# Kernel tuning notes

Measured on AMD Instinct MI355X. Metric: run time of the kernel, lower is better.

The kernel has to match this reference:

```python
import jax, jax.numpy as jnp
import numpy as np

B = 16384       # batch of peptide samples
M = 15          # max_peptide_size
R = 64          # aa_rep_size
P = 34          # number of pocket positions
F = 9           # filter_size
A = 20          # alphabet size


def setup_inputs() -> dict:
    key = jax.random.key(0)
    k1, k2, k3, k4 = jax.random.split(key, 4)
    peptide_encoding = jax.random.normal(k1, (B, M, R), dtype=jnp.float32)
    pocket_aa_idx = jax.random.randint(k2, (B, P), 0, A, dtype=jnp.int32)
    adj_mask = jax.random.randint(k3, (B, P, M), 0, 2, dtype=jnp.int32)
    # one trainable 1-D filter of length F per alphabet letter ('uniform' init)
    kernels = jax.random.uniform(k4, (A, F), dtype=jnp.float32, minval=-0.05, maxval=0.05)
    return {"peptide_encoding": peptide_encoding, "pocket_aa_idx": pocket_aa_idx,
            "adj_mask": adj_mask, "kernels": kernels}


def reference(peptide_encoding, pocket_aa_idx, adj_mask, kernels):
    # Per pocket position p of sample b: filter = kernels[pocket_aa_idx[b,p]]  [B,P,F]
    filt = kernels[pocket_aa_idx]
    # Convolution is linear, so sum the adjacent peptide-position encodings first:
    # s[b,p,r] = sum_m adj_mask[b,p,m] * peptide_encoding[b,m,r]   -> [B,P,R]
    s = jnp.einsum('bpm,bmr->bpr', adj_mask.astype(peptide_encoding.dtype), peptide_encoding)
    # Full convolution along the representation axis: output length R + F - 1
    conv1 = jax.vmap(jax.vmap(lambda a, b: jnp.convolve(a, b, mode='full')))
    out = conv1(s, filt)  # [B, P, R+F-1]
    return out
```

## Files before the change

kernel.cpp:

```cpp
#include <hip/hip_runtime.h>

#define MM 15
#define RR 64
#define PP 34
#define FF 9
#define AA 20
#define OW 72
#define SP 84
#define KS 12
#define AJ 20
#define AJROWS 48

__global__ __launch_bounds__(256)
void ppc_kernel(const float* __restrict__ pe,
                const int*   __restrict__ idx,
                const int*   __restrict__ adj,
                const float* __restrict__ kernels,
                float*       __restrict__ out)
{
    const int b = blockIdx.x;
    const int t = threadIdx.x;

    __shared__ float s_pe[MM * RR];
    __shared__ float s_kern[AA * KS];
    __shared__ float s_adjf[AJROWS * AJ];
    __shared__ int   s_idx[PP];
    __shared__ float s_s[PP * SP];

    const float* peb  = pe  + (size_t)b * (MM * RR);
    const int*   adjb = adj + (size_t)b * (PP * MM);

    if (t < (MM * RR) / 4)
        *(float4*)&s_pe[t * 4] = *(const float4*)&peb[t * 4];
    if (t < AA * FF) {
        int a = (unsigned)t / FF, j = t - a * FF;
        s_kern[a * KS + j] = kernels[t];
    }
    for (int i = t; i < PP * MM; i += 256) {
        int p = (unsigned)i / MM, m = i - p * MM;
        s_adjf[p * AJ + m] = (float)adjb[i];
    }
    for (int i = t; i < PP * 5; i += 256) {
        int p = (unsigned)i / 5, k = i - p * 5;
        s_adjf[p * AJ + MM + k] = 0.0f;
    }
    for (int i = t; i < (AJROWS - PP) * AJ; i += 256)
        s_adjf[PP * AJ + i] = 0.0f;
    if (t < PP) s_idx[t] = idx[(size_t)b * PP + t];
    for (int i = t; i < PP * 20; i += 256) {
        int p = (unsigned)i / 20, c2 = i - p * 20;
        s_s[p * SP + (c2 < 8 ? c2 : 64 + c2)] = 0.0f;
    }
    __syncthreads();

    const int c  = t & 15;
    const int q  = t >> 4;
    const int r0 = c << 2;

    {
        const float* g0 = &s_adjf[(q)      * AJ];
        const float* g1 = &s_adjf[(q + 16) * AJ];
        const float* g2 = &s_adjf[(q + 32) * AJ];
        float x0=0,y0=0,z0=0,w0=0, x1=0,y1=0,z1=0,w1=0, x2=0,y2=0,z2=0,w2=0;
        #pragma unroll
        for (int mc = 0; mc < 4; ++mc) {
            const float4 a0 = *(const float4*)&g0[mc * 4];
            const float4 a1 = *(const float4*)&g1[mc * 4];
            const float4 a2 = *(const float4*)&g2[mc * 4];
            #pragma unroll
            for (int mm = 0; mm < 4; ++mm) {
                const int m = mc * 4 + mm;
                if (m < MM) {
                    const float4 v = *(const float4*)&s_pe[m * RR + r0];
                    const float ga = (&a0.x)[mm], gb = (&a1.x)[mm], gc = (&a2.x)[mm];
                    x0 += ga*v.x; y0 += ga*v.y; z0 += ga*v.z; w0 += ga*v.w;
                    x1 += gb*v.x; y1 += gb*v.y; z1 += gb*v.z; w1 += gb*v.w;
                    x2 += gc*v.x; y2 += gc*v.y; z2 += gc*v.z; w2 += gc*v.w;
                }
            }
        }
        *(float4*)&s_s[(q)      * SP + 8 + r0] = make_float4(x0,y0,z0,w0);
        *(float4*)&s_s[(q + 16) * SP + 8 + r0] = make_float4(x1,y1,z1,w1);
        if (q + 32 < PP)
            *(float4*)&s_s[(q + 32) * SP + 8 + r0] = make_float4(x2,y2,z2,w2);
    }
    __syncthreads();

    float* outb = out + (size_t)b * (PP * OW);

    auto do_p = [&](const int p) {
        float kf[FF];
        {
            const float* kb = &s_kern[s_idx[p] * KS];
            const float4 k0 = *(const float4*)&kb[0];
            const float4 k1 = *(const float4*)&kb[4];
            kf[0]=k0.x; kf[1]=k0.y; kf[2]=k0.z; kf[3]=k0.w;
            kf[4]=k1.x; kf[5]=k1.y; kf[6]=k1.z; kf[7]=k1.w;
            kf[8]=kb[8];
        }
        const float* row = &s_s[p * SP];
        {
            float w[12];
            *(float4*)&w[0] = *(const float4*)&row[r0];
            *(float4*)&w[4] = *(const float4*)&row[r0 + 4];
            *(float4*)&w[8] = *(const float4*)&row[r0 + 8];
            float ax=0, ay=0, az=0, aw=0;
            #pragma unroll
            for (int j = 0; j < FF; ++j) {
                const float k = kf[j];
                ax += k * w[8  - j];
                ay += k * w[9  - j];
                az += k * w[10 - j];
                aw += k * w[11 - j];
            }
            *(float4*)&outb[p * OW + r0] = make_float4(ax, ay, az, aw);
        }
        if (c < 2) {
            const int o0 = 64 + r0;
            float w[12];
            *(float4*)&w[0] = *(const float4*)&row[o0];
            *(float4*)&w[4] = *(const float4*)&row[o0 + 4];
            *(float4*)&w[8] = *(const float4*)&row[o0 + 8];
            float ax=0, ay=0, az=0, aw=0;
            #pragma unroll
            for (int j = 0; j < FF; ++j) {
                const float k = kf[j];
                ax += k * w[8  - j];
                ay += k * w[9  - j];
                az += k * w[10 - j];
                aw += k * w[11 - j];
            }
            *(float4*)&outb[p * OW + o0] = make_float4(ax, ay, az, aw);
        }
    };

    do_p(q);
    do_p(q + 16);
    if (q + 32 < PP) do_p(q + 32);
}

extern "C" void kernel_launch(void* const* d_in, const int* in_sizes, int n_in,
                              void* d_out, int out_size, void* d_ws, size_t ws_size,
                              hipStream_t stream) {
    const float* pe      = (const float*)d_in[0];
    const int*   idx     = (const int*)  d_in[1];
    const int*   adj     = (const int*)  d_in[2];
    const float* kernels = (const float*)d_in[3];
    float*       out     = (float*)d_out;

    const int B = in_sizes[0] / (MM * RR);
    ppc_kernel<<<B, 256, 0, stream>>>(pe, idx, adj, kernels, out);
}
```

Before: 72.01 us.

## Remap einsum stage to one column per thread with register-cached peptide values

The adjacency-weighted sum stage is remapped. Each thread now owns one representation column r, keeps all 15 peptide values for that column in registers, and loops over the pocket rows with wavefront-uniform (broadcast) float4 reads of the adjacency row. The adjacency padding rows and padding zeroing are removed by shrinking the row stride to 16, and the halo zeroing of s_s now uses float4 stores. The aim is fewer shared-memory loads and less setup work. The trade-off is scalar rather than vectorized s_s stores in that stage, and reduced ILP per thread.

After: 76.74 us. +6.6%, slower.

```diff
diff --git a/kernel.cpp b/kernel.cpp
--- a/kernel.cpp
+++ b/kernel.cpp
@@ -8,8 +8,7 @@
 #define OW 72
 #define SP 84
 #define KS 12
-#define AJ 20
-#define AJROWS 48
+#define AJ 16
 
 __global__ __launch_bounds__(256)
 void ppc_kernel(const float* __restrict__ pe,
@@ -23,7 +22,7 @@
 
     __shared__ float s_pe[MM * RR];
     __shared__ float s_kern[AA * KS];
-    __shared__ float s_adjf[AJROWS * AJ];
+    __shared__ float s_adjf[PP * AJ];
     __shared__ int   s_idx[PP];
     __shared__ float s_s[PP * SP];
 
@@ -40,53 +39,44 @@
         int p = (unsigned)i / MM, m = i - p * MM;
         s_adjf[p * AJ + m] = (float)adjb[i];
     }
-    for (int i = t; i < PP * 5; i += 256) {
-        int p = (unsigned)i / 5, k = i - p * 5;
-        s_adjf[p * AJ + MM + k] = 0.0f;
-    }
-    for (int i = t; i < (AJROWS - PP) * AJ; i += 256)
-        s_adjf[PP * AJ + i] = 0.0f;
     if (t < PP) s_idx[t] = idx[(size_t)b * PP + t];
-    for (int i = t; i < PP * 20; i += 256) {
-        int p = (unsigned)i / 20, c2 = i - p * 20;
-        s_s[p * SP + (c2 < 8 ? c2 : 64 + c2)] = 0.0f;
+    if (t < PP * 5) {
+        int p = (unsigned)t / 5, k = t - p * 5;
+        int off = p * SP + (k < 2 ? k * 4 : 72 + (k - 2) * 4);
+        *(float4*)&s_s[off] = make_float4(0.f, 0.f, 0.f, 0.f);
     }
     __syncthreads();
 
-    const int c  = t & 15;
-    const int q  = t >> 4;
-    const int r0 = c << 2;
-
     {
-        const float* g0 = &s_adjf[(q)      * AJ];
-        const float* g1 = &s_adjf[(q + 16) * AJ];
-        const float* g2 = &s_adjf[(q + 32) * AJ];
-        float x0=0,y0=0,z0=0,w0=0, x1=0,y1=0,z1=0,w1=0, x2=0,y2=0,z2=0,w2=0;
+        const int w = t >> 6;
+        const int r = t & 63;
+        float pv[MM];
         #pragma unroll
-        for (int mc = 0; mc < 4; ++mc) {
-            const float4 a0 = *(const float4*)&g0[mc * 4];
-            const float4 a1 = *(const float4*)&g1[mc * 4];
-            const float4 a2 = *(const float4*)&g2[mc * 4];
-            #pragma unroll
-            for (int mm = 0; mm < 4; ++mm) {
-                const int m = mc * 4 + mm;
-                if (m < MM) {
-                    const float4 v = *(const float4*)&s_pe[m * RR + r0];
-                    const float ga = (&a0.x)[mm], gb = (&a1.x)[mm], gc = (&a2.x)[mm];
-                    x0 += ga*v.x; y0 += ga*v.y; z0 += ga*v.z; w0 += ga*v.w;
-                    x1 += gb*v.x; y1 += gb*v.y; z1 += gb*v.z; w1 += gb*v.w;
-                    x2 += gc*v.x; y2 += gc*v.y; z2 += gc*v.z; w2 += gc*v.w;
-                }
+        for (int m = 0; m < MM; ++m) pv[m] = s_pe[m * RR + r];
+        #pragma unroll
+        for (int j = 0; j < 9; ++j) {
+            const int p = w + 4 * j;
+            if (p < PP) {
+                const float* g = &s_adjf[p * AJ];
+                const float4 g0 = *(const float4*)&g[0];
+                const float4 g1 = *(const float4*)&g[4];
+                const float4 g2 = *(const float4*)&g[8];
+                const float4 g3 = *(const float4*)&g[12];
+                float acc;
+                acc  = g0.x * pv[0]  + g0.y * pv[1]  + g0.z * pv[2]  + g0.w * pv[3];
+                acc += g1.x * pv[4]  + g1.y * pv[5]  + g1.z * pv[6]  + g1.w * pv[7];
+                acc += g2.x * pv[8]  + g2.y * pv[9]  + g2.z * pv[10] + g2.w * pv[11];
+                acc += g3.x * pv[12] + g3.y * pv[13] + g3.z * pv[14];
+                s_s[p * SP + 8 + r] = acc;
             }
         }
-        *(float4*)&s_s[(q)      * SP + 8 + r0] = make_float4(x0,y0,z0,w0);
-        *(float4*)&s_s[(q + 16) * SP + 8 + r0] = make_float4(x1,y1,z1,w1);
-        if (q + 32 < PP)
-            *(float4*)&s_s[(q + 32) * SP + 8 + r0] = make_float4(x2,y2,z2,w2);
     }
     __syncthreads();
 
     float* outb = out + (size_t)b * (PP * OW);
+    const int c  = t & 15;
+    const int q  = t >> 4;
+    const int r0 = c << 2;
 
     auto do_p = [&](const int p) {
         float kf[FF];
```
